# Performance work log

Measured on AMD Instinct MI355X. Metric: run time of the kernel, lower is better.

## Reference

```python
import jax, jax.numpy as jnp
import numpy as np

B, D = 16384, 4096
HID = D // 2          # 2048, gate hidden
NUM_EXPERTS = 64
TOP_K = 2


def setup_inputs() -> dict:
    key = jax.random.key(0)
    ks = jax.random.split(key, 5)
    x = jax.random.normal(ks[0], (B, D), dtype=jnp.float32)
    W1 = jax.random.normal(ks[1], (D, HID), dtype=jnp.float32) * 0.02
    b1 = jnp.zeros((HID,), dtype=jnp.float32)
    W2 = jax.random.normal(ks[2], (HID, NUM_EXPERTS), dtype=jnp.float32) * 0.02
    b2 = jnp.zeros((NUM_EXPERTS,), dtype=jnp.float32)
    return {"x": x, "W1": W1, "b1": b1, "W2": W2, "b2": b2}


def reference(x, W1, b1, W2, b2):
    # gate MLP: Linear -> SiLU -> Linear
    h = jax.nn.silu(x @ W1 + b1)              # [B, HID]
    logits = h @ W2 + b2                      # [B, E]
    # top-k gating (eval mode: no noise)
    top_vals, top_idx = jax.lax.top_k(logits, TOP_K)   # [B, K]
    weights = jax.nn.softmax(top_vals, axis=-1)        # [B, K]
    # Switch-style load-balance loss: E * sum_i f_i * P_i
    probs = jax.nn.softmax(logits, axis=-1)            # [B, E]
    top1 = jnp.argmax(logits, axis=-1)                 # [B]
    freq = jnp.mean(jax.nn.one_hot(top1, NUM_EXPERTS, dtype=logits.dtype), axis=0)  # f_i
    avg_prob = jnp.mean(probs, axis=0)                 # P_i
    aux_loss = NUM_EXPERTS * jnp.sum(freq * avg_prob)
    return weights, top_idx, aux_loss
```

## Files before the change

kernel.cpp:

```cpp
#include <hip/hip_runtime.h>
#include <math.h>

#define B_ROWS 16384
#define D_IN   4096
#define HID    2048
#define NEXP   64

typedef __attribute__((ext_vector_type(8))) short short8;
typedef __attribute__((ext_vector_type(4))) float f32x4;

__device__ __forceinline__ unsigned short bf16_rne(float v) {
    unsigned int u = __float_as_uint(v);
    u += 0x7fffu + ((u >> 16) & 1u);
    return (unsigned short)(u >> 16);
}
__device__ __forceinline__ void split2(float v, unsigned short& hi, unsigned short& lo) {
    unsigned short h = bf16_rne(v);
    float hf = __uint_as_float(((unsigned int)h) << 16);
    hi = h;
    lo = bf16_rne(v - hf);
}

__global__ __launch_bounds__(256) void split_x_kernel(
    const float* __restrict__ x, unsigned short* __restrict__ hi,
    unsigned short* __restrict__ lo, int n8)
{
    int i = blockIdx.x * 256 + threadIdx.x;
    const int stride = gridDim.x * 256;
    for (; i < n8; i += stride) {
        const float4* src = reinterpret_cast<const float4*>(x + (size_t)i * 8);
        float4 v0 = src[0], v1 = src[1];
        float f[8] = {v0.x, v0.y, v0.z, v0.w, v1.x, v1.y, v1.z, v1.w};
        unsigned short h8[8], l8[8];
#pragma unroll
        for (int j = 0; j < 8; ++j) split2(f[j], h8[j], l8[j]);
        *reinterpret_cast<short8*>(hi + (size_t)i * 8) = *reinterpret_cast<short8*>(h8);
        *reinterpret_cast<short8*>(lo + (size_t)i * 8) = *reinterpret_cast<short8*>(l8);
    }
}

__global__ __launch_bounds__(256) void split_w1t_kernel(
    const float* __restrict__ W1, unsigned short* __restrict__ thi,
    unsigned short* __restrict__ tlo)
{
    __shared__ float tile[64][65];
    const int k0 = blockIdx.x * 64;
    const int n0 = blockIdx.y * 64;
    const int tid = threadIdx.x;
#pragma unroll
    for (int it = 0; it < 4; ++it) {
        const int r = it * 16 + (tid >> 4);
        const int c4 = (tid & 15) * 4;
        float4 v = *reinterpret_cast<const float4*>(&W1[(size_t)(k0 + r) * HID + n0 + c4]);
        tile[r][c4 + 0] = v.x; tile[r][c4 + 1] = v.y;
        tile[r][c4 + 2] = v.z; tile[r][c4 + 3] = v.w;
    }
    __syncthreads();
#pragma unroll
    for (int it = 0; it < 2; ++it) {
        const int idx = it * 256 + tid;
        const int n  = idx >> 3;
        const int kc = (idx & 7) * 8;
        unsigned short h8[8], l8[8];
#pragma unroll
        for (int j = 0; j < 8; ++j) split2(tile[kc + j][n], h8[j], l8[j]);
        const size_t o = (size_t)(n0 + n) * D_IN + k0 + kc;
        *reinterpret_cast<short8*>(thi + o) = *reinterpret_cast<short8*>(h8);
        *reinterpret_cast<short8*>(tlo + o) = *reinterpret_cast<short8*>(l8);
    }
}

__device__ __forceinline__ void gld16(void* lds, const void* g) {
    __builtin_amdgcn_global_load_lds(
        (const __attribute__((address_space(1))) unsigned int*)g,
        (__attribute__((address_space(3))) unsigned int*)lds, 16, 0, 0);
}

__global__ __launch_bounds__(256) void gemm1_mfma_kernel(
    const unsigned short* __restrict__ xhi, const unsigned short* __restrict__ xlo,
    const unsigned short* __restrict__ whi, const unsigned short* __restrict__ wlo,
    const float* __restrict__ b1, float* __restrict__ h)
{
    __shared__ unsigned short Ah[4096], Al[4096], Bh[4096], Bl[4096];

    const int tid  = threadIdx.x;
    const int wave = tid >> 6, lane = tid & 63;
    const int wr = wave >> 1, wc = wave & 1;

    const int bid = blockIdx.x;
    const int bx = bid & 15;
    const int by = bid >> 4;
    const int rowBase = by * 128, colBase = bx * 128;

    f32x4 acc[4][4] = {};

    const int s = lane >> 4, r16 = lane & 15;
    const int aoff = (s * 128 + wr * 64 + r16) * 8;
    const int boff = (s * 128 + wc * 64 + r16) * 8;

    for (int k0 = 0; k0 < D_IN; k0 += 32) {
        __syncthreads();
#pragma unroll
        for (int t = 0; t < 2; ++t) {
            const int dstu = (wave * 128 + t * 64) * 8;
            const size_t arow = (size_t)(rowBase + t * 64 + lane) * D_IN + k0 + wave * 8;
            const size_t brow = (size_t)(colBase + t * 64 + lane) * D_IN + k0 + wave * 8;
            gld16(&Ah[dstu], &xhi[arow]);
            gld16(&Al[dstu], &xlo[arow]);
            gld16(&Bh[dstu], &whi[brow]);
            gld16(&Bl[dstu], &wlo[brow]);
        }
        __syncthreads();

        short8 avh[4], avl[4], bvh[4], bvl[4];
#pragma unroll
        for (int mf = 0; mf < 4; ++mf) {
            avh[mf] = *reinterpret_cast<const short8*>(&Ah[aoff + mf * 128]);
            avl[mf] = *reinterpret_cast<const short8*>(&Al[aoff + mf * 128]);
        }
#pragma unroll
        for (int nf = 0; nf < 4; ++nf) {
            bvh[nf] = *reinterpret_cast<const short8*>(&Bh[boff + nf * 128]);
            bvl[nf] = *reinterpret_cast<const short8*>(&Bl[boff + nf * 128]);
        }
#pragma unroll
        for (int mf = 0; mf < 4; ++mf)
#pragma unroll
            for (int nf = 0; nf < 4; ++nf) {
                acc[mf][nf] = __builtin_amdgcn_mfma_f32_16x16x32_bf16(
                    avh[mf], bvh[nf], acc[mf][nf], 0, 0, 0);
                acc[mf][nf] = __builtin_amdgcn_mfma_f32_16x16x32_bf16(
                    avh[mf], bvl[nf], acc[mf][nf], 0, 0, 0);
                acc[mf][nf] = __builtin_amdgcn_mfma_f32_16x16x32_bf16(
                    avl[mf], bvh[nf], acc[mf][nf], 0, 0, 0);
            }
    }

    const int r4 = lane >> 4;
#pragma unroll
    for (int mf = 0; mf < 4; ++mf)
#pragma unroll
        for (int nf = 0; nf < 4; ++nf) {
            const int col = colBase + wc * 64 + nf * 16 + r16;
            const float bias = b1[col];
#pragma unroll
            for (int j = 0; j < 4; ++j) {
                const int row = rowBase + wr * 64 + mf * 16 + r4 * 4 + j;
                const float c = acc[mf][nf][j] + bias;
                h[(size_t)row * HID + col] = c / (1.f + __expf(-c));
            }
        }
}

#define BM 128
#define BN 128
#define BK 16
__global__ __launch_bounds__(256) void gemm1_silu_kernel(
    const float* __restrict__ x, const float* __restrict__ W1,
    const float* __restrict__ b1, float* __restrict__ h)
{
    __shared__ float As[BK][BM + 4];
    __shared__ float Bs[BK][BN];
    const int tid = threadIdx.x;
    const int bx = blockIdx.x, by = blockIdx.y;
    const int rowBase = by * BM, colBase = bx * BN;
    const int tx = tid & 15, ty = tid >> 4;
    float acc[8][8];
#pragma unroll
    for (int i = 0; i < 8; ++i)
#pragma unroll
        for (int j = 0; j < 8; ++j) acc[i][j] = 0.f;
    const int ar = tid >> 1, ak = (tid & 1) * 8;
    const int bk = tid >> 4, bc = tid & 15;
    for (int k0 = 0; k0 < D_IN; k0 += BK) {
        {
            const float* src = &x[(size_t)(rowBase + ar) * D_IN + k0 + ak];
            float4 v0 = *reinterpret_cast<const float4*>(src);
            float4 v1 = *reinterpret_cast<const float4*>(src + 4);
            As[ak + 0][ar] = v0.x; As[ak + 1][ar] = v0.y;
            As[ak + 2][ar] = v0.z; As[ak + 3][ar] = v0.w;
            As[ak + 4][ar] = v1.x; As[ak + 5][ar] = v1.y;
            As[ak + 6][ar] = v1.z; As[ak + 7][ar] = v1.w;
        }
        {
            const float4* s4 = reinterpret_cast<const float4*>(
                &W1[(size_t)(k0 + bk) * HID + colBase]);
            float4* d4 = reinterpret_cast<float4*>(&Bs[bk][0]);
            d4[bc] = s4[bc]; d4[bc + 16] = s4[bc + 16];
        }
        __syncthreads();
#pragma unroll
        for (int kk = 0; kk < BK; ++kk) {
            float a[8], b[8];
            *reinterpret_cast<float4*>(&a[0]) = *reinterpret_cast<const float4*>(&As[kk][ty * 8]);
            *reinterpret_cast<float4*>(&a[4]) = *reinterpret_cast<const float4*>(&As[kk][ty * 8 + 4]);
            *reinterpret_cast<float4*>(&b[0]) = *reinterpret_cast<const float4*>(&Bs[kk][tx * 8]);
            *reinterpret_cast<float4*>(&b[4]) = *reinterpret_cast<const float4*>(&Bs[kk][tx * 8 + 4]);
#pragma unroll
            for (int i = 0; i < 8; ++i)
#pragma unroll
                for (int j = 0; j < 8; ++j) acc[i][j] = fmaf(a[i], b[j], acc[i][j]);
        }
        __syncthreads();
    }
#pragma unroll
    for (int i = 0; i < 8; ++i) {
        const size_t row = (size_t)rowBase + ty * 8 + i;
        float o[8];
#pragma unroll
        for (int j = 0; j < 8; ++j) {
            float c = acc[i][j] + b1[colBase + tx * 8 + j];
            o[j] = c / (1.f + expf(-c));
        }
        float4* dst = reinterpret_cast<float4*>(&h[row * HID + colBase + tx * 8]);
        dst[0] = *reinterpret_cast<float4*>(&o[0]);
        dst[1] = *reinterpret_cast<float4*>(&o[4]);
    }
}

__global__ __launch_bounds__(256) void router_kernel(
    const float* __restrict__ h, const float* __restrict__ W2,
    const float* __restrict__ b2, float* __restrict__ out,
    float* __restrict__ gFreq, float* __restrict__ gProb)
{
    __shared__ float W2s[64][NEXP];
    __shared__ float sFreq[NEXP];
    __shared__ float sProb[NEXP];

    const int tid = threadIdx.x;
    const int lane = tid & 63;
    const int wv = tid >> 6;
    const int rowBase = blockIdx.x * 32;

    if (tid < NEXP) { sFreq[tid] = 0.f; sProb[tid] = 0.f; }

    float acc[8];
#pragma unroll
    for (int i = 0; i < 8; ++i) acc[i] = 0.f;

    const int wk = tid >> 2;
    const int wf = tid & 3;

    for (int k0 = 0; k0 < HID; k0 += 64) {
        __syncthreads();
        {
            const float4* src = reinterpret_cast<const float4*>(&W2[(size_t)(k0 + wk) * NEXP]);
            float4* dst = reinterpret_cast<float4*>(&W2s[wk][0]);
#pragma unroll
            for (int p = 0; p < 4; ++p) dst[wf + 4 * p] = src[wf + 4 * p];
        }
        __syncthreads();

#pragma unroll 2
        for (int kk4 = 0; kk4 < 16; ++kk4) {
            float4 hv[8];
#pragma unroll
            for (int i = 0; i < 8; ++i) {
                const size_t row = (size_t)rowBase + wv * 8 + i;
                hv[i] = *reinterpret_cast<const float4*>(&h[row * HID + k0 + kk4 * 4]);
            }
            {
                const float w = W2s[kk4 * 4 + 0][lane];
#pragma unroll
                for (int i = 0; i < 8; ++i) acc[i] = fmaf(hv[i].x, w, acc[i]);
            }
            {
                const float w = W2s[kk4 * 4 + 1][lane];
#pragma unroll
                for (int i = 0; i < 8; ++i) acc[i] = fmaf(hv[i].y, w, acc[i]);
            }
            {
                const float w = W2s[kk4 * 4 + 2][lane];
#pragma unroll
                for (int i = 0; i < 8; ++i) acc[i] = fmaf(hv[i].z, w, acc[i]);
            }
            {
                const float w = W2s[kk4 * 4 + 3][lane];
#pragma unroll
                for (int i = 0; i < 8; ++i) acc[i] = fmaf(hv[i].w, w, acc[i]);
            }
        }
    }

    float freqLocal = 0.f, probLocal = 0.f;
#pragma unroll
    for (int i = 0; i < 8; ++i) {
        const float v = acc[i] + b2[lane];
        float m0 = v; int i0 = lane;
#pragma unroll
        for (int off = 32; off > 0; off >>= 1) {
            float vo = __shfl_xor(m0, off);
            int   io = __shfl_xor(i0, off);
            if (vo > m0 || (vo == m0 && io < i0)) { m0 = vo; i0 = io; }
        }
        float v1 = (lane == i0) ? -3.4e38f : v;
        float m1 = v1; int i1 = lane;
#pragma unroll
        for (int off = 32; off > 0; off >>= 1) {
            float vo = __shfl_xor(m1, off);
            int   io = __shfl_xor(i1, off);
            if (vo > m1 || (vo == m1 && io < i1)) { m1 = vo; i1 = io; }
        }
        const float e = expf(v - m0);
        float sden = e;
#pragma unroll
        for (int off = 32; off > 0; off >>= 1) sden += __shfl_xor(sden, off);
        probLocal += e / sden;
        freqLocal += (lane == i0) ? 1.f : 0.f;

        if (lane == 0) {
            const size_t row = (size_t)rowBase + wv * 8 + i;
            const float e1 = expf(m1 - m0);
            const float w0 = 1.f / (1.f + e1);
            out[row * 2 + 0] = w0;
            out[row * 2 + 1] = e1 * w0;
            out[2 * B_ROWS + row * 2 + 0] = (float)i0;
            out[2 * B_ROWS + row * 2 + 1] = (float)i1;
        }
    }
    atomicAdd(&sFreq[lane], freqLocal);
    atomicAdd(&sProb[lane], probLocal);
    __syncthreads();
    if (tid < NEXP) {
        atomicAdd(&gFreq[tid], sFreq[tid]);
        atomicAdd(&gProb[tid], sProb[tid]);
    }
}

__global__ void zero_acc_kernel(float* gAcc) { gAcc[threadIdx.x] = 0.f; }

__global__ void aux_kernel(const float* __restrict__ gFreq,
                           const float* __restrict__ gProb,
                           float* __restrict__ out) {
    const int lane = threadIdx.x;
    float v = gFreq[lane] * gProb[lane];
#pragma unroll
    for (int off = 32; off > 0; off >>= 1) v += __shfl_xor(v, off);
    if (lane == 0)
        out[4 * B_ROWS] = v * ((float)NEXP / ((float)B_ROWS * (float)B_ROWS));
}

extern "C" void kernel_launch(void* const* d_in, const int* in_sizes, int n_in,
                              void* d_out, int out_size, void* d_ws, size_t ws_size,
                              hipStream_t stream) {
    const float* x  = (const float*)d_in[0];
    const float* W1 = (const float*)d_in[1];
    const float* b1 = (const float*)d_in[2];
    const float* W2 = (const float*)d_in[3];
    const float* b2 = (const float*)d_in[4];
    float* out = (float*)d_out;

    float* gFreq = (float*)d_ws;
    float* gProb = gFreq + 64;
    float* h     = (float*)((char*)d_ws + 1024);

    const size_t hBytes  = (size_t)B_ROWS * HID * 4;
    const size_t xBytes  = (size_t)B_ROWS * D_IN * 2;
    const size_t wBytes  = (size_t)HID * D_IN * 2;
    unsigned short* xhi = (unsigned short*)((char*)h + hBytes);
    unsigned short* xlo = (unsigned short*)((char*)xhi + xBytes);
    unsigned short* whi = (unsigned short*)((char*)xlo + xBytes);
    unsigned short* wlo = (unsigned short*)((char*)whi + wBytes);
    const size_t need = 1024 + hBytes + 2 * xBytes + 2 * wBytes;

    zero_acc_kernel<<<1, 128, 0, stream>>>(gFreq);

    if (ws_size >= need) {
        const int n8 = (B_ROWS * D_IN) / 8;
        split_x_kernel<<<4096, 256, 0, stream>>>(x, xhi, xlo, n8);
        dim3 gw(D_IN / 64, HID / 64);
        split_w1t_kernel<<<gw, 256, 0, stream>>>(W1, whi, wlo);
        gemm1_mfma_kernel<<<(B_ROWS / 128) * (HID / 128), 256, 0, stream>>>(
            xhi, xlo, whi, wlo, b1, h);
    } else {
        dim3 g1(HID / BN, B_ROWS / BM);
        gemm1_silu_kernel<<<g1, 256, 0, stream>>>(x, W1, b1, h);
    }

    router_kernel<<<B_ROWS / 32, 256, 0, stream>>>(h, W2, b2, out, gFreq, gProb);
    aux_kernel<<<1, NEXP, 0, stream>>>(gFreq, gProb, out);
}
```

Measured before the change: 1.886 ms.

## Rewrite split-bf16 GEMM as 256x256 tile, 4-stage pipelined 8-wave kernel

Replaces the 128x128 bf16x3 GEMM with a 256x256-tile, 512-thread kernel. It treats the three split-precision products as one long K loop of 384 steps, staged through a 4-deep LDS ring filled by global_load_lds, with explicit vmcnt waits, barriers and raised wave priority around the MFMA phases. Blocks are remapped for L2 locality. The router also drops its LDS staging of W2 and reads W2 directly from global/L1 into registers. The aim is to hide memory latency behind MFMA work and reduce synchronization cost, at the price of fragile hand-tuned wait counts and higher register pressure.

```diff
diff --git a/kernel.cpp b/kernel.cpp
--- a/kernel.cpp
+++ b/kernel.cpp
@@ -5,9 +5,14 @@
 #define D_IN   4096
 #define HID    2048
 #define NEXP   64
+#define NT     384
 
 typedef __attribute__((ext_vector_type(8))) short short8;
 typedef __attribute__((ext_vector_type(4))) float f32x4;
+
+#define VMCNT(n) asm volatile("s_waitcnt vmcnt(%0)" :: "i"(n) : "memory")
+#define GATE() do { __builtin_amdgcn_sched_barrier(0); __builtin_amdgcn_s_barrier(); \
+                    __builtin_amdgcn_sched_barrier(0); } while (0)
 
 __device__ __forceinline__ unsigned short bf16_rne(float v) {
     unsigned int u = __float_as_uint(v);
@@ -70,86 +75,122 @@
     }
 }
 
-__device__ __forceinline__ void gld16(void* lds, const void* g) {
+__device__ __forceinline__ void gld16(void* lds_p, const void* g) {
     __builtin_amdgcn_global_load_lds(
         (const __attribute__((address_space(1))) unsigned int*)g,
-        (__attribute__((address_space(3))) unsigned int*)lds, 16, 0, 0);
-}
-
-__global__ __launch_bounds__(256) void gemm1_mfma_kernel(
+        (__attribute__((address_space(3))) unsigned int*)lds_p, 16, 0, 0);
+}
+
+__global__ __launch_bounds__(512) void gemm1_8ph_kernel(
     const unsigned short* __restrict__ xhi, const unsigned short* __restrict__ xlo,
     const unsigned short* __restrict__ whi, const unsigned short* __restrict__ wlo,
     const float* __restrict__ b1, float* __restrict__ h)
 {
-    __shared__ unsigned short Ah[4096], Al[4096], Bh[4096], Bl[4096];
+    __shared__ __align__(16) unsigned short lds[4][2][1024][8];
 
     const int tid  = threadIdx.x;
-    const int wave = tid >> 6, lane = tid & 63;
-    const int wr = wave >> 1, wc = wave & 1;
+    const int lane = tid & 63, wid = tid >> 6;
+    const int wr = wid >> 2, wc = wid & 3;
 
     const int bid = blockIdx.x;
-    const int bx = bid & 15;
-    const int by = bid >> 4;
-    const int rowBase = by * 128, colBase = bx * 128;
-
-    f32x4 acc[4][4] = {};
-
-    const int s = lane >> 4, r16 = lane & 15;
-    const int aoff = (s * 128 + wr * 64 + r16) * 8;
-    const int boff = (s * 128 + wc * 64 + r16) * 8;
-
-    for (int k0 = 0; k0 < D_IN; k0 += 32) {
-        __syncthreads();
-#pragma unroll
-        for (int t = 0; t < 2; ++t) {
-            const int dstu = (wave * 128 + t * 64) * 8;
-            const size_t arow = (size_t)(rowBase + t * 64 + lane) * D_IN + k0 + wave * 8;
-            const size_t brow = (size_t)(colBase + t * 64 + lane) * D_IN + k0 + wave * 8;
-            gld16(&Ah[dstu], &xhi[arow]);
-            gld16(&Al[dstu], &xlo[arow]);
-            gld16(&Bh[dstu], &whi[brow]);
-            gld16(&Bl[dstu], &wlo[brow]);
-        }
-        __syncthreads();
-
-        short8 avh[4], avl[4], bvh[4], bvl[4];
-#pragma unroll
-        for (int mf = 0; mf < 4; ++mf) {
-            avh[mf] = *reinterpret_cast<const short8*>(&Ah[aoff + mf * 128]);
-            avl[mf] = *reinterpret_cast<const short8*>(&Al[aoff + mf * 128]);
-        }
-#pragma unroll
-        for (int nf = 0; nf < 4; ++nf) {
-            bvh[nf] = *reinterpret_cast<const short8*>(&Bh[boff + nf * 128]);
-            bvl[nf] = *reinterpret_cast<const short8*>(&Bl[boff + nf * 128]);
-        }
+    const int wg  = (bid & 7) * 64 + (bid >> 3);
+    const int rid = wg >> 3, cid = wg & 7;
+    const int rowBase = rid * 256, colBase = cid * 256;
+
+    const int sv    = tid >> 8;
+    const int rrow  = tid & 255;
+    const int ubase = tid & 448;
+
+    const int afo = ((((lane >> 4) << 8) + (wr << 7) + (lane & 15)) << 3);
+    const int bfo = ((((lane >> 4) << 8) + (wc << 6) + (lane & 15)) << 3);
+
+    f32x4 acc[8][4];
+#pragma unroll
+    for (int i = 0; i < 8; ++i)
+#pragma unroll
+        for (int j = 0; j < 4; ++j) { acc[i][j][0]=0.f; acc[i][j][1]=0.f; acc[i][j][2]=0.f; acc[i][j][3]=0.f; }
+
+    auto stage_pair = [&](int t, int ab) {
+        const int term = t >> 7;
+        const int kin  = (t & 127) << 5;
+        const unsigned short* src;
+        size_t base;
+        if (ab == 0) {
+            src  = (term < 2) ? xhi : xlo;
+            base = (size_t)(rowBase + rrow) * D_IN + kin;
+        } else {
+            src  = (term == 1) ? wlo : whi;
+            base = (size_t)(colBase + rrow) * D_IN + kin;
+        }
+        const int buf = t & 3;
+        gld16(&lds[buf][ab][ubase][0],       src + base + sv * 8);
+        gld16(&lds[buf][ab][512 + ubase][0], src + base + (2 + sv) * 8);
+    };
+
+    stage_pair(0, 0); stage_pair(0, 1);
+    stage_pair(1, 0); stage_pair(1, 1);
+    stage_pair(2, 0); stage_pair(2, 1);
+    VMCNT(8);
+    GATE();
+
+    short8 afr[8], bfr[4];
+
+    for (int t = 0; t < NT; ++t) {
+        const unsigned short* bufA = &lds[t & 3][0][0][0];
+        const unsigned short* bufB = &lds[t & 3][1][0][0];
+
+#pragma unroll
+        for (int nf = 0; nf < 4; ++nf)
+            bfr[nf] = *reinterpret_cast<const short8*>(bufB + bfo + nf * 128);
 #pragma unroll
         for (int mf = 0; mf < 4; ++mf)
-#pragma unroll
-            for (int nf = 0; nf < 4; ++nf) {
+            afr[mf] = *reinterpret_cast<const short8*>(bufA + afo + mf * 128);
+        if (t + 3 < NT) stage_pair(t + 3, 0);
+        GATE();
+        __builtin_amdgcn_s_setprio(1);
+#pragma unroll
+        for (int mf = 0; mf < 4; ++mf)
+#pragma unroll
+            for (int nf = 0; nf < 4; ++nf)
                 acc[mf][nf] = __builtin_amdgcn_mfma_f32_16x16x32_bf16(
-                    avh[mf], bvh[nf], acc[mf][nf], 0, 0, 0);
+                    afr[mf], bfr[nf], acc[mf][nf], 0, 0, 0);
+        __builtin_amdgcn_s_setprio(0);
+        GATE();
+
+#pragma unroll
+        for (int mf = 4; mf < 8; ++mf)
+            afr[mf] = *reinterpret_cast<const short8*>(bufA + afo + mf * 128);
+        if (t + 3 < NT) stage_pair(t + 3, 1);
+        GATE();
+        __builtin_amdgcn_s_setprio(1);
+#pragma unroll
+        for (int mf = 4; mf < 8; ++mf)
+#pragma unroll
+            for (int nf = 0; nf < 4; ++nf)
                 acc[mf][nf] = __builtin_amdgcn_mfma_f32_16x16x32_bf16(
-                    avh[mf], bvl[nf], acc[mf][nf], 0, 0, 0);
-                acc[mf][nf] = __builtin_amdgcn_mfma_f32_16x16x32_bf16(
-                    avl[mf], bvh[nf], acc[mf][nf], 0, 0, 0);
-            }
-    }
-
-    const int r4 = lane >> 4;
-#pragma unroll
-    for (int mf = 0; mf < 4; ++mf)
-#pragma unroll
-        for (int nf = 0; nf < 4; ++nf) {
-            const int col = colBase + wc * 64 + nf * 16 + r16;
-            const float bias = b1[col];
+                    afr[mf], bfr[nf], acc[mf][nf], 0, 0, 0);
+        __builtin_amdgcn_s_setprio(0);
+        if (t < NT - 3)       { VMCNT(8); }
+        else if (t == NT - 3) { VMCNT(4); }
+        else if (t == NT - 2) { VMCNT(0); }
+        GATE();
+    }
+
+    const int r16 = lane & 15, r4 = lane >> 4;
+#pragma unroll
+    for (int nf = 0; nf < 4; ++nf) {
+        const int col = colBase + wc * 64 + nf * 16 + r16;
+        const float bias = b1[col];
+#pragma unroll
+        for (int mf = 0; mf < 8; ++mf) {
 #pragma unroll
             for (int j = 0; j < 4; ++j) {
-                const int row = rowBase + wr * 64 + mf * 16 + r4 * 4 + j;
+                const int row = rowBase + wr * 128 + mf * 16 + r4 * 4 + j;
                 const float c = acc[mf][nf][j] + bias;
                 h[(size_t)row * HID + col] = c / (1.f + __expf(-c));
             }
         }
+    }
 }
 
 #define BM 128
@@ -218,69 +259,33 @@
     }
 }
 
-__global__ __launch_bounds__(256) void router_kernel(
+__global__ __launch_bounds__(256) void router2_kernel(
     const float* __restrict__ h, const float* __restrict__ W2,
     const float* __restrict__ b2, float* __restrict__ out,
     float* __restrict__ gFreq, float* __restrict__ gProb)
 {
-    __shared__ float W2s[64][NEXP];
-    __shared__ float sFreq[NEXP];
-    __shared__ float sProb[NEXP];
-
-    const int tid = threadIdx.x;
-    const int lane = tid & 63;
-    const int wv = tid >> 6;
-    const int rowBase = blockIdx.x * 32;
-
+    __shared__ float sFreq[NEXP], sProb[NEXP];
+    const int tid = threadIdx.x, lane = tid & 63, wv = tid >> 6;
+    const size_t rowBase = (size_t)blockIdx.x * 32 + (size_t)wv * 8;
     if (tid < NEXP) { sFreq[tid] = 0.f; sProb[tid] = 0.f; }
 
-    float acc[8];
-#pragma unroll
-    for (int i = 0; i < 8; ++i) acc[i] = 0.f;
-
-    const int wk = tid >> 2;
-    const int wf = tid & 3;
-
-    for (int k0 = 0; k0 < HID; k0 += 64) {
-        __syncthreads();
-        {
-            const float4* src = reinterpret_cast<const float4*>(&W2[(size_t)(k0 + wk) * NEXP]);
-            float4* dst = reinterpret_cast<float4*>(&W2s[wk][0]);
-#pragma unroll
-            for (int p = 0; p < 4; ++p) dst[wf + 4 * p] = src[wf + 4 * p];
-        }
-        __syncthreads();
+    float acc[8] = {0.f, 0.f, 0.f, 0.f, 0.f, 0.f, 0.f, 0.f};
 
 #pragma unroll 2
-        for (int kk4 = 0; kk4 < 16; ++kk4) {
-            float4 hv[8];
-#pragma unroll
-            for (int i = 0; i < 8; ++i) {
-                const size_t row = (size_t)rowBase + wv * 8 + i;
-                hv[i] = *reinterpret_cast<const float4*>(&h[row * HID + k0 + kk4 * 4]);
-            }
-            {
-                const float w = W2s[kk4 * 4 + 0][lane];
-#pragma unroll
-                for (int i = 0; i < 8; ++i) acc[i] = fmaf(hv[i].x, w, acc[i]);
-            }
-            {
-                const float w = W2s[kk4 * 4 + 1][lane];
-#pragma unroll
-                for (int i = 0; i < 8; ++i) acc[i] = fmaf(hv[i].y, w, acc[i]);
-            }
-            {
-                const float w = W2s[kk4 * 4 + 2][lane];
-#pragma unroll
-                for (int i = 0; i < 8; ++i) acc[i] = fmaf(hv[i].z, w, acc[i]);
-            }
-            {
-                const float w = W2s[kk4 * 4 + 3][lane];
-#pragma unroll
-                for (int i = 0; i < 8; ++i) acc[i] = fmaf(hv[i].w, w, acc[i]);
-            }
-        }
-    }
+    for (int k0 = 0; k0 < HID; k0 += 8) {
+        float w2r[8];
+#pragma unroll
+        for (int j = 0; j < 8; ++j) w2r[j] = W2[(size_t)(k0 + j) * NEXP + lane];
+#pragma unroll
+        for (int i = 0; i < 8; ++i) {
+            const float4 h0 = *reinterpret_cast<const float4*>(&h[(rowBase + i) * HID + k0]);
+            const float4 h1 = *reinterpret_cast<const float4*>(&h[(rowBase + i) * HID + k0 + 4]);
+            acc[i] += h0.x * w2r[0] + h0.y * w2r[1] + h0.z * w2r[2] + h0.w * w2r[3]
+                    + h1.x * w2r[4] + h1.y * w2r[5] + h1.z * w2r[6] + h1.w * w2r[7];
+        }
+    }
+
+    __syncthreads();
 
     float freqLocal = 0.f, probLocal = 0.f;
 #pragma unroll
@@ -309,7 +314,7 @@
         freqLocal += (lane == i0) ? 1.f : 0.f;
 
         if (lane == 0) {
-            const size_t row = (size_t)rowBase + wv * 8 + i;
+            const size_t row = rowBase + i;
             const float e1 = expf(m1 - m0);
             const float w0 = 1.f / (1.f + e1);
             out[row * 2 + 0] = w0;
@@ -354,9 +359,9 @@
     float* gProb = gFreq + 64;
     float* h     = (float*)((char*)d_ws + 1024);
 
-    const size_t hBytes  = (size_t)B_ROWS * HID * 4;
-    const size_t xBytes  = (size_t)B_ROWS * D_IN * 2;
-    const size_t wBytes  = (size_t)HID * D_IN * 2;
+    const size_t hBytes = (size_t)B_ROWS * HID * 4;
+    const size_t xBytes = (size_t)B_ROWS * D_IN * 2;
+    const size_t wBytes = (size_t)HID * D_IN * 2;
     unsigned short* xhi = (unsigned short*)((char*)h + hBytes);
     unsigned short* xlo = (unsigned short*)((char*)xhi + xBytes);
     unsigned short* whi = (unsigned short*)((char*)xlo + xBytes);
@@ -370,13 +375,12 @@
         split_x_kernel<<<4096, 256, 0, stream>>>(x, xhi, xlo, n8);
         dim3 gw(D_IN / 64, HID / 64);
         split_w1t_kernel<<<gw, 256, 0, stream>>>(W1, whi, wlo);
-        gemm1_mfma_kernel<<<(B_ROWS / 128) * (HID / 128), 256, 0, stream>>>(
-            xhi, xlo, whi, wlo, b1, h);
+        gemm1_8ph_kernel<<<512, 512, 0, stream>>>(xhi, xlo, whi, wlo, b1, h);
     } else {
         dim3 g1(HID / BN, B_ROWS / BM);
         gemm1_silu_kernel<<<g1, 256, 0, stream>>>(x, W1, b1, h);
     }
 
-    router_kernel<<<B_ROWS / 32, 256, 0, stream>>>(h, W2, b2, out, gFreq, gProb);
+    router2_kernel<<<B_ROWS / 32, 256, 0, stream>>>(h, W2, b2, out, gFreq, gProb);
     aux_kernel<<<1, NEXP, 0, stream>>>(gFreq, gProb, out);
 }
```

Measured after the change: 1.876 ms. About the same (-0.5%).
